# Optimization experiments

Measured on AMD Instinct MI355X. Metric: run time of the kernel, lower is better.

The kernel has to match this reference:

```python
import math
import jax, jax.numpy as jnp
import numpy as np

B, T, H, E, K, F = 4, 4096, 512, 8, 2, 2048
CAP_FACTOR, ROUND_TO = 0.3125, 128


def _capacity(num_tokens):
    cap = math.ceil(CAP_FACTOR * num_tokens)
    cap = ROUND_TO * math.ceil(cap / ROUND_TO)
    return max(1, min(cap, num_tokens))


def setup_inputs() -> dict:
    key = jax.random.key(0)
    k0, k1, k2, k3 = jax.random.split(key, 4)
    x = jax.random.normal(k0, (B, T, H), jnp.float32)
    router_w = jax.random.normal(k1, (H, E), jnp.float32) * 0.02
    w1 = jax.random.normal(k2, (E, H, F), jnp.float32) * (1.0 / np.sqrt(H))
    b1 = jnp.zeros((E, F), jnp.float32)
    w2 = jax.random.normal(k3, (E, F, H), jnp.float32) * (1.0 / np.sqrt(F))
    b2 = jnp.zeros((E, H), jnp.float32)
    return {"x": x, "router_w": router_w, "w1": w1, "b1": b1, "w2": w2, "b2": b2}


def reference(x, router_w, w1, b1, w2, b2):
    Bc, Tc, Hc = x.shape
    n = Bc * Tc
    cap = _capacity(n)  # static: 5120
    flat = x.reshape(n, Hc)

    # Router + top-k selection (fp32 logits, softmax over selected logits)
    logits = (flat @ router_w).astype(jnp.float32)          # [n, E]
    sel_logits, expert_idx = jax.lax.top_k(logits, K)       # [n, K]
    weights = jax.nn.softmax(sel_logits, axis=-1)           # [n, K]

    # Flatten (token, k) assignments and sort by expert (stable)
    fe = expert_idx.reshape(-1).astype(jnp.int32)           # [n*K]
    fw = weights.reshape(-1)
    tok = jnp.broadcast_to(jnp.arange(n, dtype=jnp.int32)[:, None], expert_idx.shape).reshape(-1)
    order = jnp.argsort(fe)  # jax sort is stable
    se, st, sw = fe[order], tok[order], fw[order]

    # Per-expert slot index; assignments beyond capacity are dropped
    counts = jnp.bincount(se, length=E)                     # [E]
    offsets = (jnp.cumsum(counts) - counts).astype(jnp.int32)
    slot = jnp.arange(se.shape[0], dtype=jnp.int32) - offsets[se]
    keep = slot < cap
    sw = jnp.where(keep, sw, 0.0)                           # dropped tokens contribute 0

    # Pack into fixed-capacity expert buffers (out-of-range slots dropped)
    sx = flat[st]                                           # [n*K, H]
    expert_inputs = jnp.zeros((E, cap, Hc), flat.dtype).at[se, slot].set(sx, mode='drop')

    # Grouped expert MLP: Dense(F) -> GELU -> Dense(H)
    h = jax.nn.gelu(jnp.einsum('ech,ehf->ecf', expert_inputs, w1) + b1[:, None, :])
    out = jnp.einsum('ecf,efh->ech', h, w2) + b2[:, None, :]

    # Zero invalid (unused) slots
    clipped = jnp.minimum(counts, cap)
    valid = (jnp.arange(cap, dtype=jnp.int32)[None, :] < clipped[:, None])[..., None]
    out = jnp.where(valid, out, 0)

    # Scatter-combine weighted expert outputs back to tokens
    slot_c = jnp.minimum(slot, cap - 1)                     # dropped rows have weight 0
    gathered = out[se, slot_c] * sw[:, None].astype(out.dtype)
    combined = jnp.zeros((n, Hc), out.dtype).at[st].add(gathered)
    return combined.reshape(Bc, Tc, Hc)
```

## Files before the change

### kernel.cpp

```cpp
#include <hip/hip_runtime.h>
#include <hip/hip_bf16.h>

#define NTOK 16384
#define HD   512
#define ED   8
#define FD   2048
#define CAP  5120
#define NA   32768

typedef __bf16 bf16x8 __attribute__((ext_vector_type(8)));
typedef float  f32x4  __attribute__((ext_vector_type(4)));

static constexpr size_t OFF_EIDX = 0;
static constexpr size_t OFF_WGT  = 131072;
static constexpr size_t OFF_STOK = 262144;
static constexpr size_t OFF_ASLOT= 425984;
static constexpr size_t OFF_ECNT = 557056;
static constexpr size_t OFF_W2T  = 1u << 20;
static constexpr size_t OFF_H    = OFF_W2T + (size_t)ED*HD*FD*2;
static constexpr size_t OFF_W1T  = OFF_H   + (size_t)ED*CAP*FD*2;
static constexpr size_t OFF_XBF  = OFF_W1T + (size_t)ED*FD*HD*2;
static constexpr size_t OFF_EOUT = OFF_XBF + (size_t)NTOK*HD*2;

__device__ __forceinline__ unsigned short f2bf(float f) {
    __bf16 b = (__bf16)f;
    return __builtin_bit_cast(unsigned short, b);
}
__device__ __forceinline__ unsigned short f2h(float f) {
    _Float16 h = (_Float16)f;
    return __builtin_bit_cast(unsigned short, h);
}
__device__ __forceinline__ float h2f(unsigned short u) {
    return (float)__builtin_bit_cast(_Float16, u);
}

__device__ __forceinline__ float gelu_fast(float v) {
    const float t = v * v;
    const float u = v * fmaf(t, 0.0713548214f, 1.5957691216f);
    const float e = __expf(-u);
    return v * __builtin_amdgcn_rcpf(1.f + e);
}

__global__ __launch_bounds__(256) void transpose_cast_kernel(
    const float* __restrict__ w1, unsigned short* __restrict__ w1t,
    const float* __restrict__ w2, unsigned short* __restrict__ w2t)
{
    __shared__ unsigned short tile[32][33];
    const int z = blockIdx.z;
    const bool is1 = z < ED;
    const int e = is1 ? z : z - ED;
    const int R = is1 ? HD : FD;
    const int C = is1 ? FD : HD;
    const int r0 = (is1 ? blockIdx.y : blockIdx.x) * 32;
    const int c0 = (is1 ? blockIdx.x : blockIdx.y) * 32;
    const float* in = (is1 ? w1 : w2) + (size_t)e * HD * FD;
    unsigned short* out = (is1 ? w1t : w2t) + (size_t)e * HD * FD;
    const int tr = threadIdx.x >> 3, tc = (threadIdx.x & 7) * 4;
    const float4 v = *(const float4*)(in + (size_t)(r0 + tr) * C + c0 + tc);
    tile[tr][tc + 0] = f2bf(v.x);
    tile[tr][tc + 1] = f2bf(v.y);
    tile[tr][tc + 2] = f2bf(v.z);
    tile[tr][tc + 3] = f2bf(v.w);
    __syncthreads();
    ushort4 o;
    o.x = tile[tc + 0][tr]; o.y = tile[tc + 1][tr];
    o.z = tile[tc + 2][tr]; o.w = tile[tc + 3][tr];
    *(ushort4*)(out + (size_t)(c0 + tr) * R + r0 + tc) = o;
}

__global__ __launch_bounds__(256) void router_kernel(
    const float* __restrict__ x, const float* __restrict__ rw,
    int* __restrict__ eidx, float* __restrict__ wgt,
    unsigned short* __restrict__ xbf)
{
    __shared__ float rws[HD * ED];
    const int tid = threadIdx.x;
    for (int i = tid * 4; i < HD * ED; i += 256 * 4)
        *(float4*)(rws + i) = *(const float4*)(rw + i);
    __syncthreads();

    const int wid = tid >> 6, lane = tid & 63;
    const int t = blockIdx.x * 4 + wid;
    const float* xr = x + (size_t)t * HD;

    float acc[ED];
#pragma unroll
    for (int e = 0; e < ED; e++) acc[e] = 0.f;

    float4 xv0 = *(const float4*)(xr + lane * 8);
    float4 xv1 = *(const float4*)(xr + lane * 8 + 4);
    float xv[8] = {xv0.x, xv0.y, xv0.z, xv0.w, xv1.x, xv1.y, xv1.z, xv1.w};

    union { unsigned short us[8]; uint4 v; } pk;
#pragma unroll
    for (int j = 0; j < 8; j++) pk.us[j] = f2bf(xv[j]);
    *(uint4*)(xbf + (size_t)t * HD + lane * 8) = pk.v;

#pragma unroll
    for (int j = 0; j < 8; j++) {
        const int h = lane * 8 + j;
#pragma unroll
        for (int e = 0; e < ED; e++) acc[e] += xv[j] * rws[h * ED + e];
    }
#pragma unroll
    for (int off = 32; off >= 1; off >>= 1) {
#pragma unroll
        for (int e = 0; e < ED; e++) acc[e] += __shfl_down(acc[e], off);
    }
    if (lane == 0) {
        int e0 = 0; float l0 = acc[0];
        for (int e = 1; e < ED; e++) if (acc[e] > l0) { l0 = acc[e]; e0 = e; }
        int e1 = 0; float l1 = -1e30f;
        for (int e = 0; e < ED; e++) {
            if (e == e0) continue;
            if (acc[e] > l1) { l1 = acc[e]; e1 = e; }
        }
        const float ex = expf(l1 - l0);
        const float inv = 1.f / (1.f + ex);
        eidx[t * 2 + 0] = e0;  eidx[t * 2 + 1] = e1;
        wgt [t * 2 + 0] = inv; wgt [t * 2 + 1] = ex * inv;
    }
}

__global__ __launch_bounds__(1024) void scan_kernel(
    const int* __restrict__ eidx,
    int* __restrict__ stok, int* __restrict__ aslot, int* __restrict__ ecnt)
{
    __shared__ int wcnt[32][16][ED];
    __shared__ int woff[32][16][ED];
    const int tid = threadIdx.x;
    const int lane = tid & 63, wid = tid >> 6;
    const unsigned long long below = (1ull << lane) - 1ull;

    for (int i = tid; i < ED * CAP; i += 1024) stok[i] = -1;

    for (int c = 0; c < NA / 1024; c++) {
        const int e = eidx[c * 1024 + tid];
#pragma unroll
        for (int ee = 0; ee < ED; ee++) {
            unsigned long long m = __ballot(e == ee);
            if (lane == 0) wcnt[c][wid][ee] = __popcll(m);
        }
    }
    __syncthreads();

    if (wid < ED) {
        const int e = wid;
        int carry = 0;
#pragma unroll
        for (int r = 0; r < 8; r++) {
            const int idx = r * 64 + lane;
            const int v = wcnt[idx >> 4][idx & 15][e];
            int s = v;
#pragma unroll
            for (int off = 1; off < 64; off <<= 1) {
                int u = __shfl_up(s, off);
                if (lane >= off) s += u;
            }
            woff[idx >> 4][idx & 15][e] = carry + s - v;
            carry += __shfl(s, 63);
        }
        if (lane == 0) ecnt[e] = carry < CAP ? carry : CAP;
    }
    __syncthreads();

    for (int c = 0; c < NA / 1024; c++) {
        const int a = c * 1024 + tid;
        const int e = eidx[a];
        int myrank = 0;
#pragma unroll
        for (int ee = 0; ee < ED; ee++) {
            unsigned long long m = __ballot(e == ee);
            if (ee == e) myrank = __popcll(m & below);
        }
        const int slot = woff[c][wid][e] + myrank;
        if (slot < CAP) {
            stok[e * CAP + slot] = a >> 1;
            aslot[a] = slot;
        } else {
            aslot[a] = -1;
        }
    }
}

template<int KD, int ND, int NT, bool G1>
__global__ __launch_bounds__(256) void gemm_mfma(
    const unsigned short* __restrict__ Abase,
    const unsigned short* __restrict__ Bt,
    const float* __restrict__ bias,
    const int* __restrict__ stok,
    const int* __restrict__ ecnt,
    unsigned short* __restrict__ hout)
{
    constexpr int BUFE = 128 * 32;
    __shared__ __align__(16) unsigned short As[2 * BUFE];
    __shared__ __align__(16) unsigned short Bs[2 * BUFE];

    const int tid = threadIdx.x;
    const int e  = blockIdx.x & 7;
    const int g  = blockIdx.x >> 3;
    const int n0 = (g % NT) * 128;
    const int m0 = (g / NT) * 128;

    if (m0 >= ecnt[e]) return;

    const int lane = tid & 63;
    const int wid  = tid >> 6;

    const int q  = tid & 3;
    const int r1 = tid >> 2;
    const int r2 = r1 + 64;

    size_t ai1, ai2;
    if constexpr (G1) {
        const int t1 = stok[e * CAP + m0 + r1];
        const int t2 = stok[e * CAP + m0 + r2];
        ai1 = (size_t)(t1 >= 0 ? t1 : 0);
        ai2 = (size_t)(t2 >= 0 ? t2 : 0);
    } else {
        ai1 = (size_t)(e * CAP + m0 + r1);
        ai2 = (size_t)(e * CAP + m0 + r2);
    }
    const unsigned short* arow1 = Abase + ai1 * KD + q * 8;
    const unsigned short* arow2 = Abase + ai2 * KD + q * 8;
    const unsigned short* brow1 = Bt + ((size_t)e * ND + n0 + r1) * KD + q * 8;
    const unsigned short* brow2 = Bt + ((size_t)e * ND + n0 + r2) * KD + q * 8;

    const int cSw = q ^ ((r1 >> 1) & 3);
    const int oW1 = r1 * 32 + cSw * 8;
    const int oW2 = r2 * 32 + cSw * 8;

    const int wrow = (wid & 1) * 64;
    const int wcol = (wid >> 1) * 64;
    const int l15  = lane & 15;
    const int quad = lane >> 4;
    const int xq   = quad ^ ((l15 >> 1) & 3);
    const int fA   = (wrow + l15) * 32 + xq * 8;
    const int fB   = (wcol + l15) * 32 + xq * 8;

    f32x4 acc[4][4];
#pragma unroll
    for (int i = 0; i < 4; i++)
#pragma unroll
        for (int j = 0; j < 4; j++) acc[i][j] = (f32x4)0.f;

#define COMPUTE(PBUF)                                                          \
    {                                                                          \
        const unsigned short* Ab = As + (PBUF) * BUFE;                         \
        const unsigned short* Bb = Bs + (PBUF) * BUFE;                         \
        bf16x8 af[4], bfv[4];                                                  \
        _Pragma("unroll")                                                      \
        for (int i = 0; i < 4; i++) af[i]  = *(const bf16x8*)(Ab + fA + i * 512); \
        _Pragma("unroll")                                                      \
        for (int j = 0; j < 4; j++) bfv[j] = *(const bf16x8*)(Bb + fB + j * 512); \
        _Pragma("unroll")                                                      \
        for (int i = 0; i < 4; i++)                                            \
            _Pragma("unroll")                                                  \
            for (int j = 0; j < 4; j++)                                        \
                acc[i][j] = __builtin_amdgcn_mfma_f32_16x16x32_bf16(           \
                    bfv[j], af[i], acc[i][j], 0, 0, 0);                        \
    }

#define LBAR asm volatile("s_waitcnt lgkmcnt(0)\n\ts_barrier" ::: "memory")

    float4 ra1 = *(const float4*)(arow1);
    float4 ra2 = *(const float4*)(arow2);
    float4 rb1 = *(const float4*)(brow1);
    float4 rb2 = *(const float4*)(brow2);
    *(float4*)(&As[oW1]) = ra1;
    *(float4*)(&As[oW2]) = ra2;
    *(float4*)(&Bs[oW1]) = rb1;
    *(float4*)(&Bs[oW2]) = rb2;
    if (32 < KD) {
        ra1 = *(const float4*)(arow1 + 32);
        ra2 = *(const float4*)(arow2 + 32);
        rb1 = *(const float4*)(brow1 + 32);
        rb2 = *(const float4*)(brow2 + 32);
    }
    LBAR;

    int rbuf = 0;
    for (int kc = 0; kc < KD; kc += 32) {
        const int wb = (rbuf ^ 1) * BUFE;
        if (kc + 32 < KD) {
            *(float4*)(&As[wb + oW1]) = ra1;
            *(float4*)(&As[wb + oW2]) = ra2;
            *(float4*)(&Bs[wb + oW1]) = rb1;
            *(float4*)(&Bs[wb + oW2]) = rb2;
            if (kc + 64 < KD) {
                ra1 = *(const float4*)(arow1 + kc + 64);
                ra2 = *(const float4*)(arow2 + kc + 64);
                rb1 = *(const float4*)(brow1 + kc + 64);
                rb2 = *(const float4*)(brow2 + kc + 64);
            }
        }
        COMPUTE(rbuf);
        LBAR;
        rbuf ^= 1;
    }
#undef COMPUTE
#undef LBAR

#pragma unroll
    for (int i = 0; i < 4; i++) {
        unsigned short* hrow = hout
            + ((size_t)e * CAP + m0 + wrow + i * 16 + l15) * ND
            + n0 + wcol + quad * 4;
#pragma unroll
        for (int j = 0; j < 4; j++) {
            const float4 b4 = *(const float4*)(
                bias + (size_t)e * ND + n0 + wcol + j * 16 + quad * 4);
            const float v0 = acc[i][j][0] + b4.x;
            const float v1 = acc[i][j][1] + b4.y;
            const float v2 = acc[i][j][2] + b4.z;
            const float v3 = acc[i][j][3] + b4.w;
            ushort4 o;
            if constexpr (G1) {
                o.x = f2bf(gelu_fast(v0)); o.y = f2bf(gelu_fast(v1));
                o.z = f2bf(gelu_fast(v2)); o.w = f2bf(gelu_fast(v3));
            } else {
                o.x = f2h(v0); o.y = f2h(v1); o.z = f2h(v2); o.w = f2h(v3);
            }
            *(ushort4*)(hrow + j * 16) = o;
        }
    }
}

__global__ __launch_bounds__(256) void combine_kernel(
    const unsigned short* __restrict__ eout,
    const int* __restrict__ eidx, const int* __restrict__ aslot,
    const float* __restrict__ wgt, float* __restrict__ out)
{
    const int tid = threadIdx.x;
    const int t  = blockIdx.x * 2 + (tid >> 7);
    const int h0 = (tid & 127) * 4;
    float r0 = 0.f, r1 = 0.f, r2 = 0.f, r3 = 0.f;
#pragma unroll
    for (int k = 0; k < 2; k++) {
        const int a = t * 2 + k;
        const int s = aslot[a];
        if (s >= 0) {
            const float w = wgt[a];
            const int e = eidx[a];
            const ushort4 v = *(const ushort4*)(eout + ((size_t)e * CAP + s) * HD + h0);
            r0 += w * h2f(v.x); r1 += w * h2f(v.y);
            r2 += w * h2f(v.z); r3 += w * h2f(v.w);
        }
    }
    float4 o; o.x = r0; o.y = r1; o.z = r2; o.w = r3;
    *(float4*)(out + (size_t)t * HD + h0) = o;
}

extern "C" void kernel_launch(void* const* d_in, const int* in_sizes, int n_in,
                              void* d_out, int out_size, void* d_ws, size_t ws_size,
                              hipStream_t stream)
{
    const float* x  = (const float*)d_in[0];
    const float* rw = (const float*)d_in[1];
    const float* w1 = (const float*)d_in[2];
    const float* b1 = (const float*)d_in[3];
    const float* w2 = (const float*)d_in[4];
    const float* b2 = (const float*)d_in[5];
    float* out = (float*)d_out;

    char* ws = (char*)d_ws;
    int*   eidx  = (int*)  (ws + OFF_EIDX);
    float* wgt   = (float*)(ws + OFF_WGT);
    int*   stok  = (int*)  (ws + OFF_STOK);
    int*   aslot = (int*)  (ws + OFF_ASLOT);
    int*   ecnt  = (int*)  (ws + OFF_ECNT);
    unsigned short* w2t  = (unsigned short*)(ws + OFF_W2T);
    unsigned short* hbuf = (unsigned short*)(ws + OFF_H);
    unsigned short* w1t  = (unsigned short*)(ws + OFF_W1T);
    unsigned short* xbf  = (unsigned short*)(ws + OFF_XBF);
    unsigned short* eout = (unsigned short*)(ws + OFF_EOUT);

    transpose_cast_kernel<<<dim3(FD / 32, HD / 32, 2 * ED), 256, 0, stream>>>(
        w1, w1t, w2, w2t);
    router_kernel<<<NTOK / 4, 256, 0, stream>>>(x, rw, eidx, wgt, xbf);
    scan_kernel<<<1, 1024, 0, stream>>>(eidx, stok, aslot, ecnt);

    gemm_mfma<HD, FD, FD/128, true>
        <<<8 * (FD/128) * (CAP/128), 256, 0, stream>>>(
        xbf, w1t, b1, stok, ecnt, hbuf);

    gemm_mfma<FD, HD, HD/128, false>
        <<<8 * (HD/128) * (CAP/128), 256, 0, stream>>>(
        hbuf, w2t, b2, nullptr, ecnt, eout);

    combine_kernel<<<NTOK / 2, 256, 0, stream>>>(eout, eidx, aslot, wgt, out);
}
```

Before: 454.9 us.

## Fuse weight transpose with router and split single-block scan into three kernels

Merges the weight transpose/cast and the router into one launch, using the grid z dimension to pick the role, so both run concurrently. Replaces the single 1024-thread scan block with separate count, prefix and assign kernels that run across 32 blocks, with per-wave counts and offsets kept in global workspace. This removes a serial one-block bottleneck and one launch, but adds two more launches and global round-trips for the intermediate counts.

```diff
diff --git a/kernel.cpp b/kernel.cpp
--- a/kernel.cpp
+++ b/kernel.cpp
@@ -16,6 +16,8 @@
 static constexpr size_t OFF_STOK = 262144;
 static constexpr size_t OFF_ASLOT= 425984;
 static constexpr size_t OFF_ECNT = 557056;
+static constexpr size_t OFF_GWC  = 565248;
+static constexpr size_t OFF_GWO  = 581632;
 static constexpr size_t OFF_W2T  = 1u << 20;
 static constexpr size_t OFF_H    = OFF_W2T + (size_t)ED*HD*FD*2;
 static constexpr size_t OFF_W1T  = OFF_H   + (size_t)ED*CAP*FD*2;
@@ -41,46 +43,48 @@
     return v * __builtin_amdgcn_rcpf(1.f + e);
 }
 
-__global__ __launch_bounds__(256) void transpose_cast_kernel(
+__global__ __launch_bounds__(256) void prep_kernel(
     const float* __restrict__ w1, unsigned short* __restrict__ w1t,
-    const float* __restrict__ w2, unsigned short* __restrict__ w2t)
-{
-    __shared__ unsigned short tile[32][33];
-    const int z = blockIdx.z;
-    const bool is1 = z < ED;
-    const int e = is1 ? z : z - ED;
-    const int R = is1 ? HD : FD;
-    const int C = is1 ? FD : HD;
-    const int r0 = (is1 ? blockIdx.y : blockIdx.x) * 32;
-    const int c0 = (is1 ? blockIdx.x : blockIdx.y) * 32;
-    const float* in = (is1 ? w1 : w2) + (size_t)e * HD * FD;
-    unsigned short* out = (is1 ? w1t : w2t) + (size_t)e * HD * FD;
-    const int tr = threadIdx.x >> 3, tc = (threadIdx.x & 7) * 4;
-    const float4 v = *(const float4*)(in + (size_t)(r0 + tr) * C + c0 + tc);
-    tile[tr][tc + 0] = f2bf(v.x);
-    tile[tr][tc + 1] = f2bf(v.y);
-    tile[tr][tc + 2] = f2bf(v.z);
-    tile[tr][tc + 3] = f2bf(v.w);
-    __syncthreads();
-    ushort4 o;
-    o.x = tile[tc + 0][tr]; o.y = tile[tc + 1][tr];
-    o.z = tile[tc + 2][tr]; o.w = tile[tc + 3][tr];
-    *(ushort4*)(out + (size_t)(c0 + tr) * R + r0 + tc) = o;
-}
-
-__global__ __launch_bounds__(256) void router_kernel(
-    const float* __restrict__ x, const float* __restrict__ rw,
+    const float* __restrict__ w2, unsigned short* __restrict__ w2t,
+    const float* __restrict__ x,  const float* __restrict__ rw,
     int* __restrict__ eidx, float* __restrict__ wgt,
     unsigned short* __restrict__ xbf)
 {
+    const int z = blockIdx.z;
+    const int tid = threadIdx.x;
+
+    if (z < 2 * ED) {
+        __shared__ unsigned short tile[32][33];
+        const bool is1 = z < ED;
+        const int e = is1 ? z : z - ED;
+        const int R = is1 ? HD : FD;
+        const int C = is1 ? FD : HD;
+        const int r0 = (is1 ? blockIdx.y : blockIdx.x) * 32;
+        const int c0 = (is1 ? blockIdx.x : blockIdx.y) * 32;
+        const float* in = (is1 ? w1 : w2) + (size_t)e * HD * FD;
+        unsigned short* out = (is1 ? w1t : w2t) + (size_t)e * HD * FD;
+        const int tr = tid >> 3, tc = (tid & 7) * 4;
+        const float4 v = *(const float4*)(in + (size_t)(r0 + tr) * C + c0 + tc);
+        tile[tr][tc + 0] = f2bf(v.x);
+        tile[tr][tc + 1] = f2bf(v.y);
+        tile[tr][tc + 2] = f2bf(v.z);
+        tile[tr][tc + 3] = f2bf(v.w);
+        __syncthreads();
+        ushort4 o;
+        o.x = tile[tc + 0][tr]; o.y = tile[tc + 1][tr];
+        o.z = tile[tc + 2][tr]; o.w = tile[tc + 3][tr];
+        *(ushort4*)(out + (size_t)(c0 + tr) * R + r0 + tc) = o;
+        return;
+    }
+
     __shared__ float rws[HD * ED];
-    const int tid = threadIdx.x;
     for (int i = tid * 4; i < HD * ED; i += 256 * 4)
         *(float4*)(rws + i) = *(const float4*)(rw + i);
     __syncthreads();
 
+    const int b = (z - 2 * ED) * 1024 + blockIdx.y * 64 + blockIdx.x;
     const int wid = tid >> 6, lane = tid & 63;
-    const int t = blockIdx.x * 4 + wid;
+    const int t = b * 4 + wid;
     const float* xr = x + (size_t)t * HD;
 
     float acc[ED];
@@ -122,64 +126,71 @@
     }
 }
 
-__global__ __launch_bounds__(1024) void scan_kernel(
-    const int* __restrict__ eidx,
-    int* __restrict__ stok, int* __restrict__ aslot, int* __restrict__ ecnt)
-{
-    __shared__ int wcnt[32][16][ED];
-    __shared__ int woff[32][16][ED];
+__global__ __launch_bounds__(1024) void scan_count_kernel(
+    const int* __restrict__ eidx, int* __restrict__ gwcnt,
+    int* __restrict__ stok)
+{
+    const int c = blockIdx.x;
+    const int tid = threadIdx.x;
+    const int lane = tid & 63, wid = tid >> 6;
+
+    for (int i = c * 1024 + tid; i < ED * CAP; i += 32 * 1024) stok[i] = -1;
+
+    const int e = eidx[c * 1024 + tid];
+#pragma unroll
+    for (int ee = 0; ee < ED; ee++) {
+        unsigned long long m = __ballot(e == ee);
+        if (lane == 0) gwcnt[(c * 16 + wid) * ED + ee] = __popcll(m);
+    }
+}
+
+__global__ __launch_bounds__(512) void scan_prefix_kernel(
+    const int* __restrict__ gwcnt, int* __restrict__ gwoff,
+    int* __restrict__ ecnt)
+{
+    const int tid = threadIdx.x;
+    const int lane = tid & 63, wid = tid >> 6;
+    const int e = wid;
+    int carry = 0;
+#pragma unroll
+    for (int r = 0; r < 8; r++) {
+        const int idx = r * 64 + lane;
+        const int v = gwcnt[idx * ED + e];
+        int s = v;
+#pragma unroll
+        for (int off = 1; off < 64; off <<= 1) {
+            int u = __shfl_up(s, off);
+            if (lane >= off) s += u;
+        }
+        gwoff[idx * ED + e] = carry + s - v;
+        carry += __shfl(s, 63);
+    }
+    if (lane == 0) ecnt[e] = carry < CAP ? carry : CAP;
+}
+
+__global__ __launch_bounds__(1024) void scan_assign_kernel(
+    const int* __restrict__ eidx, const int* __restrict__ gwoff,
+    int* __restrict__ stok, int* __restrict__ aslot)
+{
+    const int c = blockIdx.x;
     const int tid = threadIdx.x;
     const int lane = tid & 63, wid = tid >> 6;
     const unsigned long long below = (1ull << lane) - 1ull;
 
-    for (int i = tid; i < ED * CAP; i += 1024) stok[i] = -1;
-
-    for (int c = 0; c < NA / 1024; c++) {
-        const int e = eidx[c * 1024 + tid];
-#pragma unroll
-        for (int ee = 0; ee < ED; ee++) {
-            unsigned long long m = __ballot(e == ee);
-            if (lane == 0) wcnt[c][wid][ee] = __popcll(m);
-        }
-    }
-    __syncthreads();
-
-    if (wid < ED) {
-        const int e = wid;
-        int carry = 0;
-#pragma unroll
-        for (int r = 0; r < 8; r++) {
-            const int idx = r * 64 + lane;
-            const int v = wcnt[idx >> 4][idx & 15][e];
-            int s = v;
-#pragma unroll
-            for (int off = 1; off < 64; off <<= 1) {
-                int u = __shfl_up(s, off);
-                if (lane >= off) s += u;
-            }
-            woff[idx >> 4][idx & 15][e] = carry + s - v;
-            carry += __shfl(s, 63);
-        }
-        if (lane == 0) ecnt[e] = carry < CAP ? carry : CAP;
-    }
-    __syncthreads();
-
-    for (int c = 0; c < NA / 1024; c++) {
-        const int a = c * 1024 + tid;
-        const int e = eidx[a];
-        int myrank = 0;
-#pragma unroll
-        for (int ee = 0; ee < ED; ee++) {
-            unsigned long long m = __ballot(e == ee);
-            if (ee == e) myrank = __popcll(m & below);
-        }
-        const int slot = woff[c][wid][e] + myrank;
-        if (slot < CAP) {
-            stok[e * CAP + slot] = a >> 1;
-            aslot[a] = slot;
-        } else {
-            aslot[a] = -1;
-        }
+    const int a = c * 1024 + tid;
+    const int e = eidx[a];
+    int myrank = 0;
+#pragma unroll
+    for (int ee = 0; ee < ED; ee++) {
+        unsigned long long m = __ballot(e == ee);
+        if (ee == e) myrank = __popcll(m & below);
+    }
+    const int slot = gwoff[(c * 16 + wid) * ED + e] + myrank;
+    if (slot < CAP) {
+        stok[e * CAP + slot] = a >> 1;
+        aslot[a] = slot;
+    } else {
+        aslot[a] = -1;
     }
 }
 
@@ -369,16 +380,20 @@
     int*   stok  = (int*)  (ws + OFF_STOK);
     int*   aslot = (int*)  (ws + OFF_ASLOT);
     int*   ecnt  = (int*)  (ws + OFF_ECNT);
+    int*   gwcnt = (int*)  (ws + OFF_GWC);
+    int*   gwoff = (int*)  (ws + OFF_GWO);
     unsigned short* w2t  = (unsigned short*)(ws + OFF_W2T);
     unsigned short* hbuf = (unsigned short*)(ws + OFF_H);
     unsigned short* w1t  = (unsigned short*)(ws + OFF_W1T);
     unsigned short* xbf  = (unsigned short*)(ws + OFF_XBF);
     unsigned short* eout = (unsigned short*)(ws + OFF_EOUT);
 
-    transpose_cast_kernel<<<dim3(FD / 32, HD / 32, 2 * ED), 256, 0, stream>>>(
-        w1, w1t, w2, w2t);
-    router_kernel<<<NTOK / 4, 256, 0, stream>>>(x, rw, eidx, wgt, xbf);
-    scan_kernel<<<1, 1024, 0, stream>>>(eidx, stok, aslot, ecnt);
+    prep_kernel<<<dim3(64, 16, 2 * ED + 4), 256, 0, stream>>>(
+        w1, w1t, w2, w2t, x, rw, eidx, wgt, xbf);
+
+    scan_count_kernel <<<32, 1024, 0, stream>>>(eidx, gwcnt, stok);
+    scan_prefix_kernel<<<1, 512, 0, stream>>>(gwcnt, gwoff, ecnt);
+    scan_assign_kernel<<<32, 1024, 0, stream>>>(eidx, gwoff, stok, aslot);
 
     gemm_mfma<HD, FD, FD/128, true>
         <<<8 * (FD/128) * (CAP/128), 256, 0, stream>>>(
```

Measured after the change: 423.9 us. -6.8%, faster.
